# Kernel optimization log

Hardware: AMD Instinct MI355X
Metric: run time of the kernel (lower is better)

The kernel has to match this reference:

```python
import jax, jax.numpy as jnp
import numpy as np

BSZ, TGT, KV, D, H = 4, 512, 4096, 2048, 16
HD = D // H  # 128


def setup_inputs() -> dict:
    key = jax.random.key(0)
    ks = jax.random.split(key, 12)
    p = lambda k, shape: (jax.random.normal(k, shape, dtype=jnp.float32) * 0.02)
    return {
        "x": jax.random.normal(ks[0], (BSZ, TGT, D), dtype=jnp.float32),
        "k_cache": jax.random.normal(ks[1], (BSZ, KV, D), dtype=jnp.float32),
        "v_cache": jax.random.normal(ks[2], (BSZ, KV, D), dtype=jnp.float32),
        "attn_mask": jnp.zeros((1, 1, TGT, KV), dtype=jnp.float32),
        "wq": p(ks[3], (D, D)), "bq": jnp.zeros((D,), jnp.float32),
        "wk": p(ks[4], (D, D)), "bk": jnp.zeros((D,), jnp.float32),
        "wv": p(ks[5], (D, D)), "bv": jnp.zeros((D,), jnp.float32),
        "wo": p(ks[6], (D, D)), "bo": jnp.zeros((D,), jnp.float32),
    }


def reference(x, k_cache, v_cache, attn_mask, wq, bq, wk, bk, wv, bv, wo, bo):
    bsz, tgt_len, embed_dim = x.shape
    scale = HD ** -0.5
    # projections (torch Linear: x @ W.T + b)
    q = (x @ wq.T + bq) * scale
    k = x @ wk.T + bk
    v = x @ wv.T + bv
    # write new K/V into the last tgt_len slots of the cache
    k_cache = k_cache.at[:, -tgt_len:, :].set(k)
    v_cache = v_cache.at[:, -tgt_len:, :].set(v)
    # split heads: [b, h, s, d]
    qh = q.reshape(bsz, tgt_len, H, HD).transpose(0, 2, 1, 3)
    kh = k_cache.reshape(bsz, -1, H, HD).transpose(0, 2, 1, 3)
    vh = v_cache.reshape(bsz, -1, H, HD).transpose(0, 2, 1, 3)
    scores = jnp.einsum("bhqd,bhkd->bhqk", qh, kh) + attn_mask
    probs = jax.nn.softmax(scores, axis=-1)
    out = jnp.einsum("bhqk,bhkd->bhqd", probs, vh)
    out = out.transpose(0, 2, 1, 3).reshape(bsz, tgt_len, embed_dim)
    return (out @ wo.T + bo, k_cache, v_cache)
```

## Files before the change

### kernel.cpp

```cpp
#include <hip/hip_runtime.h>
#include <hip/hip_bf16.h>

#define BSZ 4
#define TGT 512
#define KVL 4096
#define DM  2048
#define NH  16
#define HD  128
#define QSCALE 0.08838834764831845f

typedef __bf16 bf16_t;
typedef __bf16 bf16x4 __attribute__((ext_vector_type(4)));
typedef __bf16 bf16x8 __attribute__((ext_vector_type(8)));
typedef float  f32x4  __attribute__((ext_vector_type(4)));

#define MFMA16(a,b,c) __builtin_amdgcn_mfma_f32_16x16x32_bf16((a),(b),(c),0,0,0)

#define BM 128
#define BN 128
#define BK 32
#define LDK 40

__global__ __launch_bounds__(256, 2)
void proj_qkv(const float* __restrict__ x,
              const float* __restrict__ wq, const float* __restrict__ bq,
              const float* __restrict__ wk, const float* __restrict__ bk,
              const float* __restrict__ wv, const float* __restrict__ bv,
              bf16_t* __restrict__ qb, float* __restrict__ outk, float* __restrict__ outv)
{
  const int z = blockIdx.z;
  const float* W    = (z==0)? wq : (z==1)? wk : wv;
  const float* bias = (z==0)? bq : (z==1)? bk : bv;
  const int m0 = blockIdx.y * BM, n0 = blockIdx.x * BN;
  const int tid  = threadIdx.x;
  const int lane = tid & 63, w = tid >> 6;
  const int fm = lane & 15, kg = lane >> 4;
  const int wr = (w >> 1) * 64, wc = (w & 1) * 64;
  const int ar = tid >> 3, ac = tid & 7;

  __shared__ __align__(16) bf16_t As[BM][LDK];
  __shared__ __align__(16) bf16_t Bs[BN][LDK];

  f32x4 acc[4][4];
  for (int i=0;i<4;i++) for (int j=0;j<4;j++) for (int r=0;r<4;r++) acc[i][j][r]=0.f;

  for (int k0 = 0; k0 < DM; k0 += BK) {
    #pragma unroll
    for (int p = 0; p < 4; ++p) {
      int row = ar + p*32;
      f32x4 a4f = *reinterpret_cast<const f32x4*>(&x[(size_t)(m0+row)*DM + k0 + ac*4]);
      f32x4 b4f = *reinterpret_cast<const f32x4*>(&W[(size_t)(n0+row)*DM + k0 + ac*4]);
      bf16x4 a4, b4;
      #pragma unroll
      for (int r=0;r<4;r++){ a4[r]=(bf16_t)a4f[r]; b4[r]=(bf16_t)b4f[r]; }
      *reinterpret_cast<bf16x4*>(&As[row][ac*4]) = a4;
      *reinterpret_cast<bf16x4*>(&Bs[row][ac*4]) = b4;
    }
    __syncthreads();
    bf16x8 af[4], bfr[4];
    #pragma unroll
    for (int i=0;i<4;i++){
      af[i]  = *reinterpret_cast<const bf16x8*>(&As[wr+i*16+fm][kg*8]);
      bfr[i] = *reinterpret_cast<const bf16x8*>(&Bs[wc+i*16+fm][kg*8]);
    }
    #pragma unroll
    for (int i=0;i<4;i++)
      #pragma unroll
      for (int j=0;j<4;j++)
        acc[i][j] = MFMA16(af[i], bfr[j], acc[i][j]);
    __syncthreads();
  }

  float bcol[4];
  #pragma unroll
  for (int j=0;j<4;j++) bcol[j] = bias[n0+wc+j*16+fm];
  #pragma unroll
  for (int i=0;i<4;i++)
    #pragma unroll
    for (int j=0;j<4;j++){
      const int n = n0+wc+j*16+fm;
      #pragma unroll
      for (int r=0;r<4;r++){
        const int m = m0+wr+i*16+kg*4+r;
        float v = acc[i][j][r] + bcol[j];
        if (z == 0) {
          qb[(size_t)m*DM + n] = (bf16_t)(v * QSCALE);
        } else {
          float* dst = (z==1)? outk : outv;
          const int bb = m >> 9, t = m & 511;
          dst[((size_t)bb*KVL + (KVL-TGT) + t)*DM + n] = v;
        }
      }
    }
}

__global__ __launch_bounds__(256, 2)
void out_proj(const bf16_t* __restrict__ attn, const float* __restrict__ wo,
              const float* __restrict__ bo, float* __restrict__ out)
{
  const int m0 = blockIdx.y * BM, n0 = blockIdx.x * BN;
  const int tid  = threadIdx.x;
  const int lane = tid & 63, w = tid >> 6;
  const int fm = lane & 15, kg = lane >> 4;
  const int wr = (w >> 1) * 64, wc = (w & 1) * 64;
  const int ar = tid >> 3, ac = tid & 7;

  __shared__ __align__(16) bf16_t As[BM][LDK];
  __shared__ __align__(16) bf16_t Bs[BN][LDK];

  f32x4 acc[4][4];
  for (int i=0;i<4;i++) for (int j=0;j<4;j++) for (int r=0;r<4;r++) acc[i][j][r]=0.f;

  for (int k0 = 0; k0 < DM; k0 += BK) {
    #pragma unroll
    for (int p = 0; p < 2; ++p) {
      int c = tid + p*256;
      int row = c >> 2, c8 = c & 3;
      *reinterpret_cast<bf16x8*>(&As[row][c8*8]) =
        *reinterpret_cast<const bf16x8*>(&attn[(size_t)(m0+row)*DM + k0 + c8*8]);
    }
    #pragma unroll
    for (int p = 0; p < 4; ++p) {
      int row = ar + p*32;
      f32x4 b4f = *reinterpret_cast<const f32x4*>(&wo[(size_t)(n0+row)*DM + k0 + ac*4]);
      bf16x4 b4;
      #pragma unroll
      for (int r=0;r<4;r++) b4[r]=(bf16_t)b4f[r];
      *reinterpret_cast<bf16x4*>(&Bs[row][ac*4]) = b4;
    }
    __syncthreads();
    bf16x8 af[4], bfr[4];
    #pragma unroll
    for (int i=0;i<4;i++){
      af[i]  = *reinterpret_cast<const bf16x8*>(&As[wr+i*16+fm][kg*8]);
      bfr[i] = *reinterpret_cast<const bf16x8*>(&Bs[wc+i*16+fm][kg*8]);
    }
    #pragma unroll
    for (int i=0;i<4;i++)
      #pragma unroll
      for (int j=0;j<4;j++)
        acc[i][j] = MFMA16(af[i], bfr[j], acc[i][j]);
    __syncthreads();
  }

  float bcol[4];
  #pragma unroll
  for (int j=0;j<4;j++) bcol[j] = bo[n0+wc+j*16+fm];
  #pragma unroll
  for (int i=0;i<4;i++)
    #pragma unroll
    for (int j=0;j<4;j++){
      const int n = n0+wc+j*16+fm;
      #pragma unroll
      for (int r=0;r<4;r++){
        const int m = m0+wr+i*16+kg*4+r;
        out[(size_t)m*DM + n] = acc[i][j][r] + bcol[j];
      }
    }
}

#define CHUNK 64
#define LKD 136
#define LVD 72
#define LPD 72

__global__ __launch_bounds__(256, 1)
void attn_kernel(const bf16_t* __restrict__ qb,
                 const float* __restrict__ kc,
                 const float* __restrict__ vc,
                 const float* __restrict__ mask,
                 bf16_t* __restrict__ attn)
{
  const int qt = blockIdx.x;
  const int h  = blockIdx.y;
  const int b  = blockIdx.z;
  const int tid  = threadIdx.x;
  const int lane = tid & 63, w = tid >> 6;
  const int fm = lane & 15, kg = lane >> 4;
  const int sr = tid >> 5, sc = tid & 31;

  __shared__ __align__(16) bf16_t Ks[CHUNK][LKD];
  __shared__ __align__(16) bf16_t Vt[HD][LVD];
  __shared__ __align__(16) bf16_t Ps[4][32][LPD];

  const int qbase = b*TGT + qt*128 + w*32;

  bf16x8 qf[2][4];
  #pragma unroll
  for (int mi=0;mi<2;mi++)
    #pragma unroll
    for (int kk=0;kk<4;kk++)
      qf[mi][kk] = *reinterpret_cast<const bf16x8*>(
          &qb[(size_t)(qbase + mi*16 + fm)*DM + h*HD + kk*32 + kg*8]);

  f32x4 o[2][8];
  #pragma unroll
  for (int mi=0;mi<2;mi++) for (int nt=0;nt<8;nt++) for (int r=0;r<4;r++) o[mi][nt][r]=0.f;
  float mst[2][4], lst[2][4];
  #pragma unroll
  for (int mi=0;mi<2;mi++) for (int r=0;r<4;r++){ mst[mi][r]=-1e30f; lst[mi][r]=0.f; }

  const float* kbase = kc + (size_t)b*KVL*DM + h*HD;
  const float* vbase = vc + (size_t)b*KVL*DM + h*HD;

  for (int kv0 = 0; kv0 < KVL; kv0 += CHUNK) {
    #pragma unroll
    for (int p = 0; p < 8; ++p) {
      int row = sr + p*8;
      f32x4 kv4 = *reinterpret_cast<const f32x4*>(&kbase[(size_t)(kv0+row)*DM + sc*4]);
      f32x4 vv4 = *reinterpret_cast<const f32x4*>(&vbase[(size_t)(kv0+row)*DM + sc*4]);
      bf16x4 k4;
      #pragma unroll
      for (int jj=0;jj<4;jj++) k4[jj]=(bf16_t)kv4[jj];
      *reinterpret_cast<bf16x4*>(&Ks[row][sc*4]) = k4;
      #pragma unroll
      for (int jj=0;jj<4;jj++) Vt[sc*4+jj][row] = (bf16_t)vv4[jj];
    }
    __syncthreads();

    f32x4 s[2][4];
    #pragma unroll
    for (int mi=0;mi<2;mi++) for (int nt=0;nt<4;nt++) for (int r=0;r<4;r++) s[mi][nt][r]=0.f;
    #pragma unroll
    for (int nt=0;nt<4;nt++){
      #pragma unroll
      for (int kk=0;kk<4;kk++){
        bf16x8 kf = *reinterpret_cast<const bf16x8*>(&Ks[nt*16+fm][kk*32+kg*8]);
        s[0][nt] = MFMA16(qf[0][kk], kf, s[0][nt]);
        s[1][nt] = MFMA16(qf[1][kk], kf, s[1][nt]);
      }
    }

    #pragma unroll
    for (int mi=0;mi<2;mi++){
      float pm[4][4];
      #pragma unroll
      for (int nt=0;nt<4;nt++)
        #pragma unroll
        for (int r=0;r<4;r++){
          int qrow = qt*128 + w*32 + mi*16 + kg*4 + r;
          pm[nt][r] = s[mi][nt][r] + mask[(size_t)qrow*KVL + kv0 + nt*16 + fm];
        }
      float cm[4];
      #pragma unroll
      for (int r=0;r<4;r++)
        cm[r] = fmaxf(fmaxf(pm[0][r],pm[1][r]), fmaxf(pm[2][r],pm[3][r]));
      #pragma unroll
      for (int off=1; off<16; off<<=1)
        #pragma unroll
        for (int r=0;r<4;r++) cm[r] = fmaxf(cm[r], __shfl_xor(cm[r], off, 64));
      float alpha[4], rs[4];
      #pragma unroll
      for (int r=0;r<4;r++){
        float mn = fmaxf(mst[mi][r], cm[r]);
        alpha[r] = __expf(mst[mi][r] - mn);
        mst[mi][r] = mn;
        rs[r] = 0.f;
      }
      #pragma unroll
      for (int nt=0;nt<4;nt++)
        #pragma unroll
        for (int r=0;r<4;r++){
          float p = __expf(pm[nt][r] - mst[mi][r]);
          pm[nt][r] = p; rs[r] += p;
        }
      #pragma unroll
      for (int off=1; off<16; off<<=1)
        #pragma unroll
        for (int r=0;r<4;r++) rs[r] += __shfl_xor(rs[r], off, 64);
      #pragma unroll
      for (int r=0;r<4;r++) lst[mi][r] = lst[mi][r]*alpha[r] + rs[r];
      #pragma unroll
      for (int nt=0;nt<8;nt++)
        #pragma unroll
        for (int r=0;r<4;r++) o[mi][nt][r] *= alpha[r];
      #pragma unroll
      for (int nt=0;nt<4;nt++)
        #pragma unroll
        for (int r=0;r<4;r++)
          Ps[w][mi*16 + kg*4 + r][nt*16 + fm] = (bf16_t)pm[nt][r];
    }

    #pragma unroll
    for (int ks=0; ks<2; ks++){
      bf16x8 pa0 = *reinterpret_cast<const bf16x8*>(&Ps[w][fm     ][ks*32+kg*8]);
      bf16x8 pa1 = *reinterpret_cast<const bf16x8*>(&Ps[w][16 + fm][ks*32+kg*8]);
      #pragma unroll
      for (int nt=0; nt<8; nt++){
        bf16x8 vf = *reinterpret_cast<const bf16x8*>(&Vt[nt*16+fm][ks*32+kg*8]);
        o[0][nt] = MFMA16(pa0, vf, o[0][nt]);
        o[1][nt] = MFMA16(pa1, vf, o[1][nt]);
      }
    }
    __syncthreads();
  }

  #pragma unroll
  for (int mi=0;mi<2;mi++){
    float inv[4];
    #pragma unroll
    for (int r=0;r<4;r++) inv[r] = 1.0f / lst[mi][r];
    #pragma unroll
    for (int nt=0;nt<8;nt++)
      #pragma unroll
      for (int r=0;r<4;r++){
        int m = qbase + mi*16 + kg*4 + r;
        attn[(size_t)m*DM + h*HD + nt*16 + fm] = (bf16_t)(o[mi][nt][r] * inv[r]);
      }
  }
}

extern "C" void kernel_launch(void* const* d_in, const int* in_sizes, int n_in,
                              void* d_out, int out_size, void* d_ws, size_t ws_size,
                              hipStream_t stream)
{
  const float* x    = (const float*)d_in[0];
  const float* kcin = (const float*)d_in[1];
  const float* vcin = (const float*)d_in[2];
  const float* mask = (const float*)d_in[3];
  const float* wq = (const float*)d_in[4];  const float* bq = (const float*)d_in[5];
  const float* wk = (const float*)d_in[6];  const float* bk = (const float*)d_in[7];
  const float* wv = (const float*)d_in[8];  const float* bv = (const float*)d_in[9];
  const float* wo = (const float*)d_in[10]; const float* bo = (const float*)d_in[11];

  float* out  = (float*)d_out;
  float* outk = out  + (size_t)BSZ*TGT*DM;
  float* outv = outk + (size_t)BSZ*KVL*DM;

  bf16_t* qb   = (bf16_t*)d_ws;
  bf16_t* attn = qb + (size_t)BSZ*TGT*DM;

  const size_t cache_bytes = (size_t)BSZ*KVL*DM*sizeof(float);
  hipMemcpyAsync(outk, kcin, cache_bytes, hipMemcpyDeviceToDevice, stream);
  hipMemcpyAsync(outv, vcin, cache_bytes, hipMemcpyDeviceToDevice, stream);

  proj_qkv  <<<dim3(16,16,3), 256, 0, stream>>>(x, wq,bq, wk,bk, wv,bv, qb, outk, outv);
  attn_kernel<<<dim3(4,16,4), 256, 0, stream>>>(qb, outk, outv, mask, attn);
  out_proj  <<<dim3(16,16,1), 256, 0, stream>>>(attn, wo, bo, out);
}
```

Before: 1.029 ms.

## Split attention over KV halves with combine pass, copy only old cache rows

Attention is split into two KV ranges per (batch, head, q-tile), doubling the grid from 256 to 512 blocks. Each half writes unnormalized partial outputs plus running max and sum to workspace, and a new combine kernel merges them with log-sum-exp rescaling. The two full-cache memcpys become one custom kernel that copies only the rows the projection does not overwrite, and the V transpose into shared memory is restructured so each thread reads a column and does wide bf16x8 stores. The cost is extra workspace traffic for the partials and two extra launches.

```diff
diff --git a/kernel.cpp b/kernel.cpp
--- a/kernel.cpp
+++ b/kernel.cpp
@@ -15,6 +15,25 @@
 typedef float  f32x4  __attribute__((ext_vector_type(4)));
 
 #define MFMA16(a,b,c) __builtin_amdgcn_mfma_f32_16x16x32_bf16((a),(b),(c),0,0,0)
+
+#define OLDROWS (KVL - TGT)
+#define PERB    (OLDROWS * (DM/4))
+#define PERC    (BSZ * PERB)
+
+__global__ __launch_bounds__(256)
+void cache_copy(const float* __restrict__ kcin, const float* __restrict__ vcin,
+                float* __restrict__ outk, float* __restrict__ outv)
+{
+  for (size_t i = (size_t)blockIdx.x*256 + threadIdx.x; i < 2ull*PERC;
+       i += (size_t)gridDim.x*256) {
+    const float* src; float* dst; size_t j;
+    if (i < PERC) { src = kcin; dst = outk; j = i; }
+    else          { src = vcin; dst = outv; j = i - PERC; }
+    size_t b = j / PERB;
+    size_t off = j + b * (size_t)(TGT * (DM/4));
+    reinterpret_cast<f32x4*>(dst)[off] = reinterpret_cast<const f32x4*>(src)[off];
+  }
+}
 
 #define BM 128
 #define BN 128
@@ -160,24 +179,29 @@
 }
 
 #define CHUNK 64
+#define KVSPLIT 2
+#define KVRANGE (KVL / KVSPLIT)
 #define LKD 136
 #define LVD 72
 #define LPD 72
 
-__global__ __launch_bounds__(256, 1)
-void attn_kernel(const bf16_t* __restrict__ qb,
-                 const float* __restrict__ kc,
-                 const float* __restrict__ vc,
-                 const float* __restrict__ mask,
-                 bf16_t* __restrict__ attn)
+__global__ __launch_bounds__(256, 2)
+void attn_split(const bf16_t* __restrict__ qb,
+                const float* __restrict__ kc,
+                const float* __restrict__ vc,
+                const float* __restrict__ mask,
+                float* __restrict__ Opart,
+                float* __restrict__ Mpart)
 {
   const int qt = blockIdx.x;
   const int h  = blockIdx.y;
-  const int b  = blockIdx.z;
+  const int b  = blockIdx.z >> 1;
+  const int sp = blockIdx.z & 1;
   const int tid  = threadIdx.x;
   const int lane = tid & 63, w = tid >> 6;
   const int fm = lane & 15, kg = lane >> 4;
   const int sr = tid >> 5, sc = tid & 31;
+  const int vd = tid & 127, vh = tid >> 7;
 
   __shared__ __align__(16) bf16_t Ks[CHUNK][LKD];
   __shared__ __align__(16) bf16_t Vt[HD][LVD];
@@ -202,19 +226,30 @@
 
   const float* kbase = kc + (size_t)b*KVL*DM + h*HD;
   const float* vbase = vc + (size_t)b*KVL*DM + h*HD;
-
-  for (int kv0 = 0; kv0 < KVL; kv0 += CHUNK) {
+  const int kvbeg = sp * KVRANGE;
+
+  for (int kv0 = kvbeg; kv0 < kvbeg + KVRANGE; kv0 += CHUNK) {
     #pragma unroll
     for (int p = 0; p < 8; ++p) {
       int row = sr + p*8;
       f32x4 kv4 = *reinterpret_cast<const f32x4*>(&kbase[(size_t)(kv0+row)*DM + sc*4]);
-      f32x4 vv4 = *reinterpret_cast<const f32x4*>(&vbase[(size_t)(kv0+row)*DM + sc*4]);
       bf16x4 k4;
       #pragma unroll
       for (int jj=0;jj<4;jj++) k4[jj]=(bf16_t)kv4[jj];
       *reinterpret_cast<bf16x4*>(&Ks[row][sc*4]) = k4;
-      #pragma unroll
-      for (int jj=0;jj<4;jj++) Vt[sc*4+jj][row] = (bf16_t)vv4[jj];
+    }
+    {
+      float vv[32];
+      #pragma unroll
+      for (int i=0;i<32;i++)
+        vv[i] = vbase[(size_t)(kv0 + vh*32 + i)*DM + vd];
+      #pragma unroll
+      for (int i8=0;i8<4;i8++){
+        bf16x8 v8;
+        #pragma unroll
+        for (int j=0;j<8;j++) v8[j] = (bf16_t)vv[i8*8+j];
+        *reinterpret_cast<bf16x8*>(&Vt[vd][vh*32 + i8*8]) = v8;
+      }
     }
     __syncthreads();
 
@@ -295,18 +330,57 @@
     __syncthreads();
   }
 
-  #pragma unroll
-  for (int mi=0;mi<2;mi++){
-    float inv[4];
-    #pragma unroll
-    for (int r=0;r<4;r++) inv[r] = 1.0f / lst[mi][r];
+  const int pidx = (b*NH + h)*4 + qt;
+  float* obuf = Opart + ((size_t)sp*256 + pidx)*16384;
+  #pragma unroll
+  for (int mi=0;mi<2;mi++)
     #pragma unroll
     for (int nt=0;nt<8;nt++)
       #pragma unroll
       for (int r=0;r<4;r++){
-        int m = qbase + mi*16 + kg*4 + r;
-        attn[(size_t)m*DM + h*HD + nt*16 + fm] = (bf16_t)(o[mi][nt][r] * inv[r]);
-      }
+        int qrl = w*32 + mi*16 + kg*4 + r;
+        obuf[(size_t)qrl*HD + nt*16 + fm] = o[mi][nt][r];
+      }
+  if (fm == 0) {
+    float* mbuf = Mpart + ((size_t)sp*256 + pidx)*256;
+    #pragma unroll
+    for (int mi=0;mi<2;mi++)
+      #pragma unroll
+      for (int r=0;r<4;r++){
+        int qrl = w*32 + mi*16 + kg*4 + r;
+        mbuf[qrl*2 + 0] = mst[mi][r];
+        mbuf[qrl*2 + 1] = lst[mi][r];
+      }
+  }
+}
+
+__global__ __launch_bounds__(256)
+void attn_combine(const float* __restrict__ Opart, const float* __restrict__ Mpart,
+                  bf16_t* __restrict__ attn)
+{
+  const int pidx = blockIdx.x;
+  const int b  = pidx >> 6;
+  const int h  = (pidx >> 2) & 15;
+  const int qt = pidx & 3;
+  const float* o0 = Opart + (size_t)pidx*16384;
+  const float* o1 = Opart + (size_t)(256 + pidx)*16384;
+  const float* m0b = Mpart + (size_t)pidx*256;
+  const float* m1b = Mpart + (size_t)(256 + pidx)*256;
+
+  for (int e = threadIdx.x; e < 4096; e += 256) {
+    int qrow = e >> 5, c4 = e & 31;
+    float m0 = m0b[qrow*2], l0 = m0b[qrow*2+1];
+    float m1 = m1b[qrow*2], l1 = m1b[qrow*2+1];
+    float mm = fmaxf(m0, m1);
+    float s0 = __expf(m0 - mm), s1 = __expf(m1 - mm);
+    float inv = 1.0f / (l0*s0 + l1*s1);
+    f32x4 a = *reinterpret_cast<const f32x4*>(&o0[qrow*HD + c4*4]);
+    f32x4 c = *reinterpret_cast<const f32x4*>(&o1[qrow*HD + c4*4]);
+    bf16x4 r;
+    #pragma unroll
+    for (int j=0;j<4;j++) r[j] = (bf16_t)((a[j]*s0 + c[j]*s1) * inv);
+    *reinterpret_cast<bf16x4*>(
+        &attn[(size_t)(b*TGT + qt*128 + qrow)*DM + h*HD + c4*4]) = r;
   }
 }
 
@@ -327,14 +401,14 @@
   float* outk = out  + (size_t)BSZ*TGT*DM;
   float* outv = outk + (size_t)BSZ*KVL*DM;
 
-  bf16_t* qb   = (bf16_t*)d_ws;
-  bf16_t* attn = qb + (size_t)BSZ*TGT*DM;
-
-  const size_t cache_bytes = (size_t)BSZ*KVL*DM*sizeof(float);
-  hipMemcpyAsync(outk, kcin, cache_bytes, hipMemcpyDeviceToDevice, stream);
-  hipMemcpyAsync(outv, vcin, cache_bytes, hipMemcpyDeviceToDevice, stream);
-
-  proj_qkv  <<<dim3(16,16,3), 256, 0, stream>>>(x, wq,bq, wk,bk, wv,bv, qb, outk, outv);
-  attn_kernel<<<dim3(4,16,4), 256, 0, stream>>>(qb, outk, outv, mask, attn);
-  out_proj  <<<dim3(16,16,1), 256, 0, stream>>>(attn, wo, bo, out);
-}
+  bf16_t* qb    = (bf16_t*)d_ws;
+  bf16_t* attn  = qb + (size_t)BSZ*TGT*DM;
+  float*  Opart = (float*)((char*)d_ws + (16ull<<20));
+  float*  Mpart = Opart + (size_t)512*16384;
+
+  cache_copy <<<7168, 256, 0, stream>>>(kcin, vcin, outk, outv);
+  proj_qkv   <<<dim3(16,16,3), 256, 0, stream>>>(x, wq,bq, wk,bk, wv,bv, qb, outk, outv);
+  attn_split <<<dim3(4,16,8), 256, 0, stream>>>(qb, outk, outv, mask, Opart, Mpart);
+  attn_combine<<<256, 256, 0, stream>>>(Opart, Mpart, attn);
+  out_proj   <<<dim3(16,16,1), 256, 0, stream>>>(attn, wo, bo, out);
+}
```

Result: faster. 869.2 us (-15.5%).
